# Kernel optimization log

Measured on AMD Instinct MI355X. Metric: run time of the kernel, lower is better.

The kernel has to match this reference:

```python
import jax, jax.numpy as jnp
import numpy as np

EMBED, HEADS, LEVELS, POINTS = 256, 8, 3, 4
HD = EMBED // HEADS
SHAPES = [(200, 200), (100, 100), (50, 50)]


def layer_norm(x, g, b, eps=1e-5):
    m = x.mean(-1, keepdims=True)
    v = ((x - m) ** 2).mean(-1, keepdims=True)
    return (x - m) * jax.lax.rsqrt(v + eps) * g + b


def bilinear_sample(v, loc, H, W):
    """v: (bs, H*W, heads, hd); loc: (bs, nq, heads, P, 2) normalized to [0,1].
    Matches F.grid_sample(bilinear, align_corners=False, padding_mode='zeros')
    applied to grid = 2*loc - 1. Returns (bs, nq, heads, P, hd)."""
    bs, nq, heads, P, _ = loc.shape
    hd = v.shape[-1]
    x = loc[..., 0] * W - 0.5
    y = loc[..., 1] * H - 0.5
    x0 = jnp.floor(x); y0 = jnp.floor(y)
    tx = x - x0; ty = y - y0
    x0i = x0.astype(jnp.int32); y0i = y0.astype(jnp.int32)
    vT = v.transpose(0, 2, 1, 3)  # (bs, heads, HW, hd)
    out = jnp.zeros((bs, heads, nq * P, hd), v.dtype)
    for dy, wy in ((0, 1.0 - ty), (1, ty)):
        for dx, wx in ((0, 1.0 - tx), (1, tx)):
            xi = x0i + dx; yi = y0i + dy
            valid = (xi >= 0) & (xi < W) & (yi >= 0) & (yi < H)
            idx = jnp.clip(yi, 0, H - 1) * W + jnp.clip(xi, 0, W - 1)
            w = (wx * wy * valid).transpose(0, 2, 1, 3).reshape(bs, heads, nq * P)
            idxT = idx.transpose(0, 2, 1, 3).reshape(bs, heads, nq * P)
            g = jnp.take_along_axis(vT, idxT[..., None], axis=2)  # (bs,heads,nqP,hd)
            out = out + w[..., None] * g
    return out.reshape(bs, heads, nq, P, hd).transpose(0, 2, 1, 3, 4)


def reference(query, value, query_pos, ref_pts, spatial_shapes, level_start_index,
              norm1_g, norm1_b, W_off, b_off, W_attn, b_attn, W_val, b_val,
              W_out, b_out, norm2_g, norm2_b, W1, b1, W2, b2):
    shapes = np.asarray(spatial_shapes)
    bs, nq, _ = query.shape
    # --- MultiScaleDeformableAttention on norm1(query) ---
    q = layer_norm(query, norm1_g, norm1_b)
    identity = q
    qp = q + query_pos
    offsets = (qp @ W_off + b_off).reshape(bs, nq, HEADS, LEVELS, POINTS, 2)
    aw = (qp @ W_attn + b_attn).reshape(bs, nq, HEADS, LEVELS * POINTS)
    aw = jax.nn.softmax(aw, axis=-1).reshape(bs, nq, HEADS, LEVELS, POINTS)
    v = (value @ W_val + b_val).reshape(bs, -1, HEADS, HD)
    # offset normalizer is (W, H) per level
    normalizer = jnp.stack([spatial_shapes[:, 1], spatial_shapes[:, 0]], -1).astype(query.dtype)
    loc = ref_pts[:, :, None, :, None, :] + offsets / normalizer[None, None, None, :, None, :]
    out = jnp.zeros((bs, nq, HEADS, HD), query.dtype)
    start = 0
    for l in range(LEVELS):
        H, W = int(shapes[l, 0]), int(shapes[l, 1])
        vl = v[:, start:start + H * W]
        s = bilinear_sample(vl, loc[:, :, :, l], H, W)  # (bs,nq,heads,P,hd)
        out = out + jnp.einsum('bqhpd,bqhp->bqhd', s, aw[:, :, :, l])
        start += H * W
    attn_out = out.reshape(bs, nq, EMBED) @ W_out + b_out + identity
    x = query + attn_out
    # --- FFN ---
    h = layer_norm(x, norm2_g, norm2_b)
    ffn = jax.nn.gelu(h @ W1 + b1, approximate=False) @ W2 + b2
    return x + ffn


def setup_inputs() -> dict:
    key = jax.random.key(0)
    ks = jax.random.split(key, 16)
    bs, nq = 1, 40000
    nv = sum(h * w for h, w in SHAPES)
    d = EMBED
    inp = {
        'query': jax.random.normal(ks[0], (bs, nq, d), jnp.float32),
        'value': jax.random.normal(ks[1], (bs, nv, d), jnp.float32),
        'query_pos': jax.random.normal(ks[2], (bs, nq, d), jnp.float32),
        'ref_pts': jax.random.uniform(ks[3], (bs, nq, LEVELS, 2), jnp.float32),
        'spatial_shapes': jnp.array(SHAPES, dtype=jnp.int32),
        'level_start_index': jnp.array(np.cumsum([0] + [h * w for h, w in SHAPES[:-1]]), dtype=jnp.int32),
    }
    s = 1.0 / np.sqrt(d)
    inp.update({
        'norm1_g': jnp.ones((d,), jnp.float32), 'norm1_b': jnp.zeros((d,), jnp.float32),
        'W_off': jax.random.normal(ks[4], (d, HEADS * LEVELS * POINTS * 2), jnp.float32) * 0.01,
        'b_off': jax.random.normal(ks[5], (HEADS * LEVELS * POINTS * 2,), jnp.float32) * 0.5,
        'W_attn': jax.random.normal(ks[6], (d, HEADS * LEVELS * POINTS), jnp.float32) * s,
        'b_attn': jnp.zeros((HEADS * LEVELS * POINTS,), jnp.float32),
        'W_val': jax.random.normal(ks[7], (d, d), jnp.float32) * s,
        'b_val': jnp.zeros((d,), jnp.float32),
        'W_out': jax.random.normal(ks[8], (d, d), jnp.float32) * s,
        'b_out': jnp.zeros((d,), jnp.float32),
        'norm2_g': jnp.ones((d,), jnp.float32), 'norm2_b': jnp.zeros((d,), jnp.float32),
        'W1': jax.random.normal(ks[9], (d, 4 * d), jnp.float32) * s,
        'b1': jnp.zeros((4 * d,), jnp.float32),
        'W2': jax.random.normal(ks[10], (4 * d, d), jnp.float32) / np.sqrt(4 * d),
        'b2': jnp.zeros((d,), jnp.float32),
    })
    return inp
```

## Files before the change

kernel.cpp:

```cpp
#include <hip/hip_runtime.h>
#include <hip/hip_bf16.h>
#include <math.h>

#define NQ 40000
#define NV 52500
#define D 256
#define NHEAD 8
#define HD 32
#define GUARD 256

using bf16x8 = __attribute__((ext_vector_type(8))) short;
using f32x4  = __attribute__((ext_vector_type(4))) float;
typedef int v2i32 __attribute__((ext_vector_type(2)));

__device__ __forceinline__ short f2bf(float f) {
  union { __hip_bfloat16 h; short s; } u;
  u.h = __float2bfloat16(f);
  return u.s;
}
__device__ __forceinline__ float bf2f(unsigned short s) {
  return __uint_as_float((unsigned)s << 16);
}
__device__ __forceinline__ unsigned pack2(float lo, float hi) {
  return (unsigned)(unsigned short)f2bf(lo) |
         ((unsigned)(unsigned short)f2bf(hi) << 16);
}
__device__ __forceinline__ void gload16(const void* g, void* l) {
  __builtin_amdgcn_global_load_lds(
      (const __attribute__((address_space(1))) unsigned int*)g,
      (__attribute__((address_space(3))) unsigned int*)l, 16, 0, 0);
}

template<int IMM>
__device__ __forceinline__ float swz_add(float x) {
  return x + __int_as_float(__builtin_amdgcn_ds_swizzle(__float_as_int(x), IMM));
}
__device__ __forceinline__ float xor16_add(float x) {
#if __has_builtin(__builtin_amdgcn_permlane16_swap)
  v2i32 r = __builtin_amdgcn_permlane16_swap(__float_as_int(x), __float_as_int(x), false, false);
  return __int_as_float(r[0]) + __int_as_float(r[1]);
#else
  return x + __shfl_xor(x, 16);
#endif
}
__device__ __forceinline__ float xor32_add(float x) {
#if __has_builtin(__builtin_amdgcn_permlane32_swap)
  v2i32 r = __builtin_amdgcn_permlane32_swap(__float_as_int(x), __float_as_int(x), false, false);
  return __int_as_float(r[0]) + __int_as_float(r[1]);
#else
  return x + __shfl_xor(x, 32);
#endif
}

__global__ __launch_bounds__(256) void k_wt(const float* __restrict__ Wm,
                                            short* __restrict__ WT, int K, int N) {
  int idx = blockIdx.x * 256 + threadIdx.x;
  if (idx >= N * K) return;
  int n = idx / K, k = idx - n * K;
  WT[idx] = f2bf(Wm[(size_t)k * N + n]);
}

__global__ void k_catbias(const float* __restrict__ a, const float* __restrict__ b,
                          float* __restrict__ o) {
  int i = threadIdx.x;
  if (i < 192) o[i] = a[i];
  else if (i < 288) o[i] = b[i - 192];
}

__global__ __launch_bounds__(256) void k_ln1(const float* __restrict__ qin,
                                             const float* __restrict__ qpos,
                                             const float* __restrict__ g,
                                             const float* __restrict__ b,
                                             float* __restrict__ id_out,
                                             short* __restrict__ qp_out) {
  int wave = threadIdx.x >> 6;
  int lane = threadIdx.x & 63;
  int row  = blockIdx.x * 4 + wave;
  float4 x = ((const float4*)(qin + (size_t)row * D))[lane];
  float s  = x.x + x.y + x.z + x.w;
  float ss = x.x*x.x + x.y*x.y + x.z*x.z + x.w*x.w;
  for (int o = 32; o > 0; o >>= 1) { s += __shfl_down(s, o); ss += __shfl_down(ss, o); }
  s  = __shfl(s, 0);
  ss = __shfl(ss, 0);
  float m   = s * (1.0f / 256.0f);
  float var = ss * (1.0f / 256.0f) - m * m;
  float rs  = rsqrtf(var + 1e-5f);
  float4 gg = ((const float4*)g)[lane];
  float4 bb = ((const float4*)b)[lane];
  float4 qn;
  qn.x = (x.x - m) * rs * gg.x + bb.x;
  qn.y = (x.y - m) * rs * gg.y + bb.y;
  qn.z = (x.z - m) * rs * gg.z + bb.z;
  qn.w = (x.w - m) * rs * gg.w + bb.w;
  ((float4*)(id_out + (size_t)row * D))[lane] = qn;
  float4 p = ((const float4*)(qpos + (size_t)row * D))[lane];
  short4 o;
  o.x = f2bf(qn.x + p.x); o.y = f2bf(qn.y + p.y);
  o.z = f2bf(qn.z + p.z); o.w = f2bf(qn.w + p.w);
  ((short4*)(qp_out + (size_t)row * D))[lane] = o;
}

__global__ __launch_bounds__(256) void k_ln2(const float* __restrict__ xin,
                                             const float* __restrict__ g,
                                             const float* __restrict__ b,
                                             short* __restrict__ h_out) {
  int wave = threadIdx.x >> 6;
  int lane = threadIdx.x & 63;
  int row  = blockIdx.x * 4 + wave;
  float4 x = ((const float4*)(xin + (size_t)row * D))[lane];
  float s  = x.x + x.y + x.z + x.w;
  float ss = x.x*x.x + x.y*x.y + x.z*x.z + x.w*x.w;
  for (int o = 32; o > 0; o >>= 1) { s += __shfl_down(s, o); ss += __shfl_down(ss, o); }
  s  = __shfl(s, 0);
  ss = __shfl(ss, 0);
  float m   = s * (1.0f / 256.0f);
  float var = ss * (1.0f / 256.0f) - m * m;
  float rs  = rsqrtf(var + 1e-5f);
  float4 gg = ((const float4*)g)[lane];
  float4 bb = ((const float4*)b)[lane];
  short4 o;
  o.x = f2bf((x.x - m) * rs * gg.x + bb.x);
  o.y = f2bf((x.y - m) * rs * gg.y + bb.y);
  o.z = f2bf((x.z - m) * rs * gg.z + bb.z);
  o.w = f2bf((x.w - m) * rs * gg.w + bb.w);
  ((short4*)(h_out + (size_t)row * D))[lane] = o;
}

template<int EPI, int CVTA, int K>
__global__ __launch_bounds__(256) void k_gemm(const void* __restrict__ Ain,
                                              const short* __restrict__ WT,
                                              const float* __restrict__ bias,
                                              float* __restrict__ Cf,
                                              short* __restrict__ Cb,
                                              const float* __restrict__ R1,
                                              const float* __restrict__ R2,
                                              int M, int N) {
  constexpr int NT = K / 32;
  __shared__ short Al[3][4096];
  __shared__ short Bl[3][4096];
  const int tid = threadIdx.x;

  const int nbx = gridDim.x;
  const int nwg = nbx * gridDim.y;
  int flat = blockIdx.y * nbx + blockIdx.x;
  {
    int xcd = flat & 7, pos = flat >> 3;
    int qq = nwg >> 3, rr = nwg & 7;
    flat = (xcd < rr ? xcd * (qq + 1) : rr * (qq + 1) + (xcd - rr) * qq) + pos;
  }
  const int n0 = (flat % nbx) * 128, m0 = (flat / nbx) * 128;

  const int w = tid >> 6, l = tid & 63;
  const int wm = (w >> 1) * 64, wn = (w & 1) * 64;
  const int lr = l & 15;

  const int c0s = w * 2, c1s = c0s + 1;
  const int sr = l >> 2;
  const int sg = (((l & 3) ^ ((l >> 3) & 3)) << 3);
  const int ar0 = min(m0 + c0s * 16 + sr, M - 1);
  const int ar1 = min(m0 + c1s * 16 + sr, M - 1);
  const int br0 = min(n0 + c0s * 16 + sr, N - 1);
  const int br1 = min(n0 + c1s * 16 + sr, N - 1);
  const short* bP0 = WT + (size_t)br0 * K + sg;
  const short* bP1 = WT + (size_t)br1 * K + sg;
  const short* aP0 = (const short*)Ain + (size_t)ar0 * K + sg;
  const short* aP1 = (const short*)Ain + (size_t)ar1 * K + sg;
  const float* aF0 = (const float*)Ain + (size_t)ar0 * K + sg;
  const float* aF1 = (const float*)Ain + (size_t)ar1 * K + sg;
  short* wD0 = &Al[0][(c0s * 16 + sr) * 32 + ((l & 3) << 3)];
  short* wD1 = &Al[0][(c1s * 16 + sr) * 32 + ((l & 3) << 3)];

  const int fsw = (((l >> 4) ^ ((l >> 1) & 3)) << 3);
  const int aRd = (wm + lr) * 32 + fsw;
  const int bRd = (wn + lr) * 32 + fsw;

  f32x4 acc[4][4];
#pragma unroll
  for (int i = 0; i < 4; ++i)
#pragma unroll
    for (int j = 0; j < 4; ++j) acc[i][j] = (f32x4){0, 0, 0, 0};

  if (CVTA) {
    {
      float4 f00 = *(const float4*)(aF0);
      float4 f01 = *(const float4*)(aF0 + 4);
      float4 f10 = *(const float4*)(aF1);
      float4 f11 = *(const float4*)(aF1 + 4);
      int4 p0, p1;
      p0.x = pack2(f00.x, f00.y); p0.y = pack2(f00.z, f00.w);
      p0.z = pack2(f01.x, f01.y); p0.w = pack2(f01.z, f01.w);
      p1.x = pack2(f10.x, f10.y); p1.y = pack2(f10.z, f10.w);
      p1.z = pack2(f11.x, f11.y); p1.w = pack2(f11.z, f11.w);
      *(int4*)wD0 = p0;
      *(int4*)wD1 = p1;
      gload16(bP0, &Bl[0][c0s * 512]);
      gload16(bP1, &Bl[0][c1s * 512]);
      __syncthreads();
    }
#pragma unroll 2
    for (int t = 0; t < NT - 1; ++t) {
      const int buf = t & 1, nbuf = buf ^ 1;
      const int kn = (t + 1) * 32;
      float4 f00 = *(const float4*)(aF0 + kn);
      float4 f01 = *(const float4*)(aF0 + kn + 4);
      float4 f10 = *(const float4*)(aF1 + kn);
      float4 f11 = *(const float4*)(aF1 + kn + 4);
      gload16(bP0 + kn, &Bl[nbuf][c0s * 512]);
      gload16(bP1 + kn, &Bl[nbuf][c1s * 512]);

      bf16x8 af[4], bfr[4];
#pragma unroll
      for (int i = 0; i < 4; ++i) {
        af[i]  = *(const bf16x8*)&Al[buf][aRd + i * 512];
        bfr[i] = *(const bf16x8*)&Bl[buf][bRd + i * 512];
      }
#pragma unroll
      for (int i = 0; i < 4; ++i)
#pragma unroll
        for (int j = 0; j < 4; ++j)
          acc[i][j] = __builtin_amdgcn_mfma_f32_16x16x32_bf16(af[i], bfr[j], acc[i][j], 0, 0, 0);

      int4 p0, p1;
      p0.x = pack2(f00.x, f00.y); p0.y = pack2(f00.z, f00.w);
      p0.z = pack2(f01.x, f01.y); p0.w = pack2(f01.z, f01.w);
      p1.x = pack2(f10.x, f10.y); p1.y = pack2(f10.z, f10.w);
      p1.z = pack2(f11.x, f11.y); p1.w = pack2(f11.z, f11.w);
      *(int4*)(wD0 + nbuf * 4096) = p0;
      *(int4*)(wD1 + nbuf * 4096) = p1;
      __syncthreads();
    }
    {
      const int buf = (NT - 1) & 1;
      bf16x8 af[4], bfr[4];
#pragma unroll
      for (int i = 0; i < 4; ++i) {
        af[i]  = *(const bf16x8*)&Al[buf][aRd + i * 512];
        bfr[i] = *(const bf16x8*)&Bl[buf][bRd + i * 512];
      }
#pragma unroll
      for (int i = 0; i < 4; ++i)
#pragma unroll
        for (int j = 0; j < 4; ++j)
          acc[i][j] = __builtin_amdgcn_mfma_f32_16x16x32_bf16(af[i], bfr[j], acc[i][j], 0, 0, 0);
    }
  } else {
    gload16(aP0, &Al[0][c0s * 512]);
    gload16(aP1, &Al[0][c1s * 512]);
    gload16(bP0, &Bl[0][c0s * 512]);
    gload16(bP1, &Bl[0][c1s * 512]);
    if (NT > 1) {
      gload16(aP0 + 32, &Al[1][c0s * 512]);
      gload16(aP1 + 32, &Al[1][c1s * 512]);
      gload16(bP0 + 32, &Bl[1][c0s * 512]);
      gload16(bP1 + 32, &Bl[1][c1s * 512]);
    }
#pragma unroll
    for (int t = 0; t < NT; ++t) {
      const int buf = t % 3;
      if (t + 1 < NT) asm volatile("s_waitcnt vmcnt(4)" ::: "memory");
      else            asm volatile("s_waitcnt vmcnt(0)" ::: "memory");
      __builtin_amdgcn_s_barrier();
      __builtin_amdgcn_sched_barrier(0);
      if (t + 2 < NT) {
        const int kn = (t + 2) * 32, nb = (t + 2) % 3;
        gload16(aP0 + kn, &Al[nb][c0s * 512]);
        gload16(aP1 + kn, &Al[nb][c1s * 512]);
        gload16(bP0 + kn, &Bl[nb][c0s * 512]);
        gload16(bP1 + kn, &Bl[nb][c1s * 512]);
      }
      bf16x8 af[4], bfr[4];
#pragma unroll
      for (int i = 0; i < 4; ++i) {
        af[i]  = *(const bf16x8*)&Al[buf][aRd + i * 512];
        bfr[i] = *(const bf16x8*)&Bl[buf][bRd + i * 512];
      }
#pragma unroll
      for (int i = 0; i < 4; ++i)
#pragma unroll
        for (int j = 0; j < 4; ++j)
          acc[i][j] = __builtin_amdgcn_mfma_f32_16x16x32_bf16(af[i], bfr[j], acc[i][j], 0, 0, 0);
    }
  }

  __syncthreads();
  float* scratch = (float*)&Al[0][0];
  const int wrow = (w >> 1) * 16;
  const int rl2 = tid >> 3;
  const int cc0 = (tid & 7) * 16;
  const bool colok = (n0 + cc0) < N;
  float bsv[16];
#pragma unroll
  for (int c = 0; c < 4; ++c) {
    float4 bv = {0, 0, 0, 0};
    if (colok) bv = *(const float4*)&bias[n0 + cc0 + c * 4];
    bsv[c*4+0] = bv.x; bsv[c*4+1] = bv.y; bsv[c*4+2] = bv.z; bsv[c*4+3] = bv.w;
  }
#pragma unroll
  for (int i = 0; i < 4; ++i) {
#pragma unroll
    for (int j = 0; j < 4; ++j) {
      const int col = wn + j * 16 + (l & 15);
      const int rbase = wrow + ((l >> 4) << 2);
#pragma unroll
      for (int r = 0; r < 4; ++r)
        scratch[(rbase + r) * 140 + col] = acc[i][j][r];
    }
    __syncthreads();
    const int grow = m0 + 16 * i + (rl2 < 16 ? rl2 : 48 + rl2);
    if (colok && grow < M) {
      const size_t base = (size_t)grow * N + n0 + cc0;
      float v16[16];
#pragma unroll
      for (int c = 0; c < 4; ++c) {
        float4 vv = *(const float4*)&scratch[rl2 * 140 + cc0 + c * 4];
        v16[c*4+0] = vv.x + bsv[c*4+0];
        v16[c*4+1] = vv.y + bsv[c*4+1];
        v16[c*4+2] = vv.z + bsv[c*4+2];
        v16[c*4+3] = vv.w + bsv[c*4+3];
      }
      if (EPI == 0) {
#pragma unroll
        for (int c = 0; c < 4; ++c)
          *(float4*)&Cf[base + c * 4] =
              (float4){v16[c*4], v16[c*4+1], v16[c*4+2], v16[c*4+3]};
      } else if (EPI == 1) {
        uint4 o0, o1;
        unsigned pk[8];
#pragma unroll
        for (int c = 0; c < 8; ++c) {
          float a0 = v16[2*c], a1 = v16[2*c+1];
          float u0 = a0 * (2.3021178f + 0.1029445f * a0 * a0);
          float u1 = a1 * (2.3021178f + 0.1029445f * a1 * a1);
          float g0 = a0 - a0 / (1.0f + exp2f(u0));
          float g1 = a1 - a1 / (1.0f + exp2f(u1));
          pk[c] = pack2(g0, g1);
        }
        o0 = (uint4){pk[0], pk[1], pk[2], pk[3]};
        o1 = (uint4){pk[4], pk[5], pk[6], pk[7]};
        *(uint4*)&Cb[base] = o0;
        *(uint4*)&Cb[base + 8] = o1;
      } else if (EPI == 2) {
#pragma unroll
        for (int c = 0; c < 4; ++c) {
          float4 r1 = *(const float4*)&R1[base + c * 4];
          float4 r2 = *(const float4*)&R2[base + c * 4];
          *(float4*)&Cf[base + c * 4] =
              (float4){v16[c*4] + r1.x + r2.x, v16[c*4+1] + r1.y + r2.y,
                       v16[c*4+2] + r1.z + r2.z, v16[c*4+3] + r1.w + r2.w};
        }
      } else if (EPI == 3) {
#pragma unroll
        for (int c = 0; c < 4; ++c) {
          float4 cur = *(const float4*)&Cf[base + c * 4];
          *(float4*)&Cf[base + c * 4] =
              (float4){cur.x + v16[c*4], cur.y + v16[c*4+1],
                       cur.z + v16[c*4+2], cur.w + v16[c*4+3]};
        }
      } else {
        uint4 o0 = (uint4){pack2(v16[0], v16[1]), pack2(v16[2], v16[3]),
                           pack2(v16[4], v16[5]), pack2(v16[6], v16[7])};
        uint4 o1 = (uint4){pack2(v16[8], v16[9]), pack2(v16[10], v16[11]),
                           pack2(v16[12], v16[13]), pack2(v16[14], v16[15])};
        *(uint4*)&Cb[base] = o0;
        *(uint4*)&Cb[base + 8] = o1;
      }
    }
    __syncthreads();
  }
}

__global__ __launch_bounds__(256) void k_post(const unsigned short* __restrict__ res,
                                              const float* __restrict__ refp,
                                              int* __restrict__ idxA,
                                              unsigned short* __restrict__ wA) {
  int t = blockIdx.x * 256 + threadIdx.x;
  if (t >= NQ * 8) return;
  int q = t >> 3, h = t & 7;
  const unsigned short* rr = res + (size_t)q * 288;
  const unsigned short* lg = rr + 192 + h * 12;
  float lf[12];
#pragma unroll
  for (int i = 0; i < 12; ++i) lf[i] = bf2f(lg[i]);
  float mx = lf[0];
#pragma unroll
  for (int i = 1; i < 12; ++i) mx = fmaxf(mx, lf[i]);
  float e[12]; float sum = 0.0f;
#pragma unroll
  for (int i = 0; i < 12; ++i) { e[i] = expf(lf[i] - mx); sum += e[i]; }
  float inv = 1.0f / sum;

  const float dims[3] = {200.0f, 100.0f, 50.0f};
  const int   sts[3]  = {0, 40000, 50000};
#pragma unroll
  for (int l = 0; l < 3; ++l) {
    const int W = (int)dims[l];
    const float fW = dims[l];
    float rx = refp[((size_t)q * 3 + l) * 2 + 0];
    float ry = refp[((size_t)q * 3 + l) * 2 + 1];
    float invd = 1.0f / fW;
#pragma unroll
    for (int p = 0; p < 4; ++p) {
      int j = ((h * 3 + l) * 4 + p) * 2;
      float lx = rx + bf2f(rr[j + 0]) * invd;
      float ly = ry + bf2f(rr[j + 1]) * invd;
      float fx = lx * fW - 0.5f;
      float fy = ly * fW - 0.5f;
      float x0f = floorf(fx), y0f = floorf(fy);
      float tx = fx - x0f, ty = fy - y0f;
      int x0 = (int)x0f, y0 = (int)y0f;
      bool vx0 = (unsigned)x0       < (unsigned)W;
      bool vx1 = (unsigned)(x0 + 1) < (unsigned)W;
      bool vy0 = (unsigned)y0       < (unsigned)W;
      bool vy1 = (unsigned)(y0 + 1) < (unsigned)W;
      float a = e[l * 4 + p] * inv;
      float w00 = (vx0 && vy0) ? a * (1.0f - tx) * (1.0f - ty) : 0.0f;
      float w01 = (vx1 && vy0) ? a * tx * (1.0f - ty) : 0.0f;
      float w10 = (vx0 && vy1) ? a * (1.0f - tx) * ty : 0.0f;
      float w11 = (vx1 && vy1) ? a * tx * ty : 0.0f;
      int pidx = t * 12 + l * 4 + p;
      idxA[pidx] = sts[l] + y0 * W + x0;
      short4 wpk;
      wpk.x = f2bf(w00); wpk.y = f2bf(w01);
      wpk.z = f2bf(w10); wpk.w = f2bf(w11);
      *(short4*)(wA + (size_t)pidx * 4) = wpk;
    }
  }
}

__global__ __launch_bounds__(256) void k_sample(const short* __restrict__ vprojG,
                                                const int* __restrict__ idxA,
                                                const unsigned short* __restrict__ wA,
                                                short* __restrict__ smp) {
  const int lane = threadIdx.x & 63;
  const int qh   = blockIdx.x * 4 + (threadIdx.x >> 6);
  const int h = qh & 7;
  const int pg  = lane >> 4;
  const int tap = (lane >> 2) & 3;
  const int cq  = lane & 3;
  const int dy = tap >> 1, dx = tap & 1;
  const short* vb = vprojG + (size_t)GUARD * D + h * HD + cq * 8;

  float acc[8];
#pragma unroll
  for (int j = 0; j < 8; ++j) acc[j] = 0.0f;

  const int Dim[3] = {200, 100, 50};
#pragma unroll
  for (int l = 0; l < 3; ++l) {
    const int W = Dim[l];
    const int tapoff = dy * W + dx;
    int pidx = qh * 12 + l * 4 + pg;
    int idx = idxA[pidx] + tapoff;
    float wgt = __uint_as_float((unsigned)wA[(size_t)pidx * 4 + tap] << 16);
    uint4 v = *(const uint4*)(vb + (ptrdiff_t)idx * D);
    acc[0] = fmaf(wgt, __uint_as_float(v.x << 16),        acc[0]);
    acc[1] = fmaf(wgt, __uint_as_float(v.x & 0xffff0000u), acc[1]);
    acc[2] = fmaf(wgt, __uint_as_float(v.y << 16),        acc[2]);
    acc[3] = fmaf(wgt, __uint_as_float(v.y & 0xffff0000u), acc[3]);
    acc[4] = fmaf(wgt, __uint_as_float(v.z << 16),        acc[4]);
    acc[5] = fmaf(wgt, __uint_as_float(v.z & 0xffff0000u), acc[5]);
    acc[6] = fmaf(wgt, __uint_as_float(v.w << 16),        acc[6]);
    acc[7] = fmaf(wgt, __uint_as_float(v.w & 0xffff0000u), acc[7]);
  }

#pragma unroll
  for (int j = 0; j < 8; ++j) {
    float a = swz_add<0x101F>(acc[j]);
    a = swz_add<0x201F>(a);
    a = xor16_add(a);
    acc[j] = xor32_add(a);
  }

  if (lane < 4) {
    uint4 o;
    o.x = pack2(acc[0], acc[1]);
    o.y = pack2(acc[2], acc[3]);
    o.z = pack2(acc[4], acc[5]);
    o.w = pack2(acc[6], acc[7]);
    *(uint4*)(smp + (size_t)qh * HD + cq * 8) = o;
  }
}

extern "C" void kernel_launch(void* const* d_in, const int* in_sizes, int n_in,
                              void* d_out, int out_size, void* d_ws, size_t ws_size,
                              hipStream_t stream) {
  const float* query  = (const float*)d_in[0];
  const float* value  = (const float*)d_in[1];
  const float* qpos   = (const float*)d_in[2];
  const float* refp   = (const float*)d_in[3];
  const float* n1g = (const float*)d_in[6];
  const float* n1b = (const float*)d_in[7];
  const float* Woff = (const float*)d_in[8];
  const float* boff = (const float*)d_in[9];
  const float* Wattn = (const float*)d_in[10];
  const float* battn = (const float*)d_in[11];
  const float* Wval = (const float*)d_in[12];
  const float* bval = (const float*)d_in[13];
  const float* Wout = (const float*)d_in[14];
  const float* bout = (const float*)d_in[15];
  const float* n2g = (const float*)d_in[16];
  const float* n2b = (const float*)d_in[17];
  const float* W1 = (const float*)d_in[18];
  const float* b1 = (const float*)d_in[19];
  const float* W2 = (const float*)d_in[20];
  const float* b2 = (const float*)d_in[21];

  float* out = (float*)d_out;
  char* Wb = (char*)d_ws;

  short* qp_bf   = (short*)Wb;
  float* iden    = (float*)(Wb + 20480000);
  int*   idxA    = (int*)(Wb + 61440000);
  unsigned short* wA = (unsigned short*)(Wb + 76800000);
  short* res_bf  = (short*)(Wb + 107520000);
  short* vprjG   = (short*)(Wb + 107520000);
  short* vprj_bf = (short*)(Wb + 107520000 + GUARD * D * 2);
  short* h_bf    = (short*)(Wb + 107520000);
  short* smp_bf  = (short*)(Wb + 134662144);
  short* mid_bf  = (short*)Wb;
  char*  Wbase   = Wb + 155142144;
  short* WT288   = (short*)(Wbase);
  short* WTval   = (short*)(Wbase + 147456);
  short* WTout   = (short*)(Wbase + 278528);
  short* WT1     = (short*)(Wbase + 409600);
  short* WT2     = (short*)(Wbase + 933888);
  float* bias288 = (float*)(Wbase + 1458176);

  k_wt<<<(192 * 256 + 255) / 256, 256, 0, stream>>>(Woff, WT288, 256, 192);
  k_wt<<<(96 * 256 + 255) / 256, 256, 0, stream>>>(Wattn, WT288 + 192 * 256, 256, 96);
  k_wt<<<(256 * 256 + 255) / 256, 256, 0, stream>>>(Wval, WTval, 256, 256);
  k_wt<<<(256 * 256 + 255) / 256, 256, 0, stream>>>(Wout, WTout, 256, 256);
  k_wt<<<(1024 * 256 + 255) / 256, 256, 0, stream>>>(W1, WT1, 256, 1024);
  k_wt<<<(256 * 1024 + 255) / 256, 256, 0, stream>>>(W2, WT2, 1024, 256);
  k_catbias<<<1, 320, 0, stream>>>(boff, battn, bias288);

  k_ln1<<<NQ / 4, 256, 0, stream>>>(query, qpos, n1g, n1b, iden, qp_bf);

  k_gemm<4,0,256><<<dim3(3, (NQ + 127) / 128), 256, 0, stream>>>(
      qp_bf, WT288, bias288, nullptr, res_bf, nullptr, nullptr, NQ, 288);
  k_post<<<(NQ * 8 + 255) / 256, 256, 0, stream>>>(
      (const unsigned short*)res_bf, refp, idxA, wA);

  k_gemm<4,1,256><<<dim3(2, (NV + 127) / 128), 256, 0, stream>>>(
      value, WTval, bval, nullptr, vprj_bf, nullptr, nullptr, NV, 256);

  k_sample<<<NQ * NHEAD / 4, 256, 0, stream>>>(vprjG, idxA, wA, smp_bf);

  k_gemm<2,0,256><<<dim3(2, (NQ + 127) / 128), 256, 0, stream>>>(
      smp_bf, WTout, bout, out, nullptr, query, iden, NQ, 256);

  k_ln2<<<NQ / 4, 256, 0, stream>>>(out, n2g, n2b, h_bf);

  k_gemm<1,0,256><<<dim3(8, (NQ + 127) / 128), 256, 0, stream>>>(
      h_bf, WT1, b1, nullptr, mid_bf, nullptr, nullptr, NQ, 1024);

  k_gemm<3,0,1024><<<dim3(2, (NQ + 127) / 128), 256, 0, stream>>>(
      mid_bf, WT2, b2, out, nullptr, nullptr, nullptr, NQ, 256);
}
```

Measured before the change: 379.3 us.

## Merge weight prep kernels, store identity as bf16, and restructure sampling lanes

The six weight-transpose launches and the bias-concat launch become one k_prep launch, which cuts launch overhead. The LayerNorm identity is now stored as bf16 instead of fp32, and a new GEMM epilogue (EPI 5) reads it back as bf16. This halves that residual's write and read traffic but adds rounding error to the residual path. The sampling kernel now gives each 16-lane group one query-head that loops over all 12 points, instead of spreading points across lane groups, so it needs only the two swizzle reductions and no permlane reductions.

```diff
diff --git a/kernel.cpp b/kernel.cpp
--- a/kernel.cpp
+++ b/kernel.cpp
@@ -35,43 +35,51 @@
 __device__ __forceinline__ float swz_add(float x) {
   return x + __int_as_float(__builtin_amdgcn_ds_swizzle(__float_as_int(x), IMM));
 }
-__device__ __forceinline__ float xor16_add(float x) {
-#if __has_builtin(__builtin_amdgcn_permlane16_swap)
-  v2i32 r = __builtin_amdgcn_permlane16_swap(__float_as_int(x), __float_as_int(x), false, false);
-  return __int_as_float(r[0]) + __int_as_float(r[1]);
-#else
-  return x + __shfl_xor(x, 16);
-#endif
-}
-__device__ __forceinline__ float xor32_add(float x) {
-#if __has_builtin(__builtin_amdgcn_permlane32_swap)
-  v2i32 r = __builtin_amdgcn_permlane32_swap(__float_as_int(x), __float_as_int(x), false, false);
-  return __int_as_float(r[0]) + __int_as_float(r[1]);
-#else
-  return x + __shfl_xor(x, 32);
-#endif
-}
-
-__global__ __launch_bounds__(256) void k_wt(const float* __restrict__ Wm,
-                                            short* __restrict__ WT, int K, int N) {
+
+__global__ __launch_bounds__(256) void k_prep(const float* __restrict__ Woff,
+                                              const float* __restrict__ Wattn,
+                                              const float* __restrict__ Wval,
+                                              const float* __restrict__ Wout,
+                                              const float* __restrict__ W1,
+                                              const float* __restrict__ W2,
+                                              const float* __restrict__ boff,
+                                              const float* __restrict__ battn,
+                                              short* __restrict__ WT288,
+                                              short* __restrict__ WTval,
+                                              short* __restrict__ WTout,
+                                              short* __restrict__ WT1,
+                                              short* __restrict__ WT2,
+                                              float* __restrict__ bias288) {
   int idx = blockIdx.x * 256 + threadIdx.x;
-  if (idx >= N * K) return;
-  int n = idx / K, k = idx - n * K;
-  WT[idx] = f2bf(Wm[(size_t)k * N + n]);
-}
-
-__global__ void k_catbias(const float* __restrict__ a, const float* __restrict__ b,
-                          float* __restrict__ o) {
-  int i = threadIdx.x;
-  if (i < 192) o[i] = a[i];
-  else if (i < 288) o[i] = b[i - 192];
+  if (idx < 49152) {
+    int n = idx >> 8, k = idx & 255;
+    WT288[idx] = f2bf(Woff[k * 192 + n]);
+  } else if (idx < 73728) {
+    int li = idx - 49152; int n = li >> 8, k = li & 255;
+    WT288[49152 + li] = f2bf(Wattn[k * 96 + n]);
+  } else if (idx < 139264) {
+    int li = idx - 73728; int n = li >> 8, k = li & 255;
+    WTval[li] = f2bf(Wval[k * 256 + n]);
+  } else if (idx < 204800) {
+    int li = idx - 139264; int n = li >> 8, k = li & 255;
+    WTout[li] = f2bf(Wout[k * 256 + n]);
+  } else if (idx < 466944) {
+    int li = idx - 204800; int n = li >> 8, k = li & 255;
+    WT1[li] = f2bf(W1[k * 1024 + n]);
+  } else if (idx < 729088) {
+    int li = idx - 466944; int n = li >> 10, k = li & 1023;
+    WT2[li] = f2bf(W2[k * 256 + n]);
+  } else if (idx < 729376) {
+    int i = idx - 729088;
+    bias288[i] = (i < 192) ? boff[i] : battn[i - 192];
+  }
 }
 
 __global__ __launch_bounds__(256) void k_ln1(const float* __restrict__ qin,
                                              const float* __restrict__ qpos,
                                              const float* __restrict__ g,
                                              const float* __restrict__ b,
-                                             float* __restrict__ id_out,
+                                             short* __restrict__ id_out,
                                              short* __restrict__ qp_out) {
   int wave = threadIdx.x >> 6;
   int lane = threadIdx.x & 63;
@@ -92,7 +100,9 @@
   qn.y = (x.y - m) * rs * gg.y + bb.y;
   qn.z = (x.z - m) * rs * gg.z + bb.z;
   qn.w = (x.w - m) * rs * gg.w + bb.w;
-  ((float4*)(id_out + (size_t)row * D))[lane] = qn;
+  short4 io;
+  io.x = f2bf(qn.x); io.y = f2bf(qn.y); io.z = f2bf(qn.z); io.w = f2bf(qn.w);
+  ((short4*)(id_out + (size_t)row * D))[lane] = io;
   float4 p = ((const float4*)(qpos + (size_t)row * D))[lane];
   short4 o;
   o.x = f2bf(qn.x + p.x); o.y = f2bf(qn.y + p.y);
@@ -284,6 +294,7 @@
 
   __syncthreads();
   float* scratch = (float*)&Al[0][0];
+  const unsigned short* R2b = (const unsigned short*)R2;
   const int wrow = (w >> 1) * 16;
   const int rl2 = tid >> 3;
   const int cc0 = (tid & 7) * 16;
@@ -324,7 +335,6 @@
           *(float4*)&Cf[base + c * 4] =
               (float4){v16[c*4], v16[c*4+1], v16[c*4+2], v16[c*4+3]};
       } else if (EPI == 1) {
-        uint4 o0, o1;
         unsigned pk[8];
 #pragma unroll
         for (int c = 0; c < 8; ++c) {
@@ -335,18 +345,24 @@
           float g1 = a1 - a1 / (1.0f + exp2f(u1));
           pk[c] = pack2(g0, g1);
         }
-        o0 = (uint4){pk[0], pk[1], pk[2], pk[3]};
-        o1 = (uint4){pk[4], pk[5], pk[6], pk[7]};
-        *(uint4*)&Cb[base] = o0;
-        *(uint4*)&Cb[base + 8] = o1;
-      } else if (EPI == 2) {
+        *(uint4*)&Cb[base] = (uint4){pk[0], pk[1], pk[2], pk[3]};
+        *(uint4*)&Cb[base + 8] = (uint4){pk[4], pk[5], pk[6], pk[7]};
+      } else if (EPI == 5) {
+        uint4 rb0 = *(const uint4*)&R2b[base];
+        uint4 rb1 = *(const uint4*)&R2b[base + 8];
+        unsigned rw[8] = {rb0.x, rb0.y, rb0.z, rb0.w, rb1.x, rb1.y, rb1.z, rb1.w};
+        float r2v[16];
+#pragma unroll
+        for (int c = 0; c < 8; ++c) {
+          r2v[2*c]   = __uint_as_float(rw[c] << 16);
+          r2v[2*c+1] = __uint_as_float(rw[c] & 0xffff0000u);
+        }
 #pragma unroll
         for (int c = 0; c < 4; ++c) {
           float4 r1 = *(const float4*)&R1[base + c * 4];
-          float4 r2 = *(const float4*)&R2[base + c * 4];
           *(float4*)&Cf[base + c * 4] =
-              (float4){v16[c*4] + r1.x + r2.x, v16[c*4+1] + r1.y + r2.y,
-                       v16[c*4+2] + r1.z + r2.z, v16[c*4+3] + r1.w + r2.w};
+              (float4){v16[c*4] + r1.x + r2v[c*4], v16[c*4+1] + r1.y + r2v[c*4+1],
+                       v16[c*4+2] + r1.z + r2v[c*4+2], v16[c*4+3] + r1.w + r2v[c*4+3]};
         }
       } else if (EPI == 3) {
 #pragma unroll
@@ -432,13 +448,13 @@
                                                 const unsigned short* __restrict__ wA,
                                                 short* __restrict__ smp) {
   const int lane = threadIdx.x & 63;
-  const int qh   = blockIdx.x * 4 + (threadIdx.x >> 6);
+  const int qh   = blockIdx.x * 16 + (threadIdx.x >> 6) * 4 + (lane >> 4);
+  const int tap  = (lane >> 2) & 3;
+  const int cq   = lane & 3;
   const int h = qh & 7;
-  const int pg  = lane >> 4;
-  const int tap = (lane >> 2) & 3;
-  const int cq  = lane & 3;
   const int dy = tap >> 1, dx = tap & 1;
   const short* vb = vprojG + (size_t)GUARD * D + h * HD + cq * 8;
+  const int pbase = qh * 12;
 
   float acc[8];
 #pragma unroll
@@ -446,12 +462,12 @@
 
   const int Dim[3] = {200, 100, 50};
 #pragma unroll
-  for (int l = 0; l < 3; ++l) {
-    const int W = Dim[l];
+  for (int it = 0; it < 12; ++it) {
+    const int W = Dim[it >> 2];
     const int tapoff = dy * W + dx;
-    int pidx = qh * 12 + l * 4 + pg;
+    int pidx = pbase + it;
     int idx = idxA[pidx] + tapoff;
-    float wgt = __uint_as_float((unsigned)wA[(size_t)pidx * 4 + tap] << 16);
+    float wgt = bf2f(wA[(size_t)pidx * 4 + tap]);
     uint4 v = *(const uint4*)(vb + (ptrdiff_t)idx * D);
     acc[0] = fmaf(wgt, __uint_as_float(v.x << 16),        acc[0]);
     acc[1] = fmaf(wgt, __uint_as_float(v.x & 0xffff0000u), acc[1]);
@@ -466,12 +482,10 @@
 #pragma unroll
   for (int j = 0; j < 8; ++j) {
     float a = swz_add<0x101F>(acc[j]);
-    a = swz_add<0x201F>(a);
-    a = xor16_add(a);
-    acc[j] = xor32_add(a);
-  }
-
-  if (lane < 4) {
+    acc[j] = swz_add<0x201F>(a);
+  }
+
+  if (tap == 0) {
     uint4 o;
     o.x = pack2(acc[0], acc[1]);
     o.y = pack2(acc[2], acc[3]);
@@ -509,7 +523,7 @@
   char* Wb = (char*)d_ws;
 
   short* qp_bf   = (short*)Wb;
-  float* iden    = (float*)(Wb + 20480000);
+  short* iden_bf = (short*)(Wb + 20480000);
   int*   idxA    = (int*)(Wb + 61440000);
   unsigned short* wA = (unsigned short*)(Wb + 76800000);
   short* res_bf  = (short*)(Wb + 107520000);
@@ -526,15 +540,11 @@
   short* WT2     = (short*)(Wbase + 933888);
   float* bias288 = (float*)(Wbase + 1458176);
 
-  k_wt<<<(192 * 256 + 255) / 256, 256, 0, stream>>>(Woff, WT288, 256, 192);
-  k_wt<<<(96 * 256 + 255) / 256, 256, 0, stream>>>(Wattn, WT288 + 192 * 256, 256, 96);
-  k_wt<<<(256 * 256 + 255) / 256, 256, 0, stream>>>(Wval, WTval, 256, 256);
-  k_wt<<<(256 * 256 + 255) / 256, 256, 0, stream>>>(Wout, WTout, 256, 256);
-  k_wt<<<(1024 * 256 + 255) / 256, 256, 0, stream>>>(W1, WT1, 256, 1024);
-  k_wt<<<(256 * 1024 + 255) / 256, 256, 0, stream>>>(W2, WT2, 1024, 256);
-  k_catbias<<<1, 320, 0, stream>>>(boff, battn, bias288);
-
-  k_ln1<<<NQ / 4, 256, 0, stream>>>(query, qpos, n1g, n1b, iden, qp_bf);
+  k_prep<<<(729376 + 255) / 256, 256, 0, stream>>>(
+      Woff, Wattn, Wval, Wout, W1, W2, boff, battn,
+      WT288, WTval, WTout, WT1, WT2, bias288);
+
+  k_ln1<<<NQ / 4, 256, 0, stream>>>(query, qpos, n1g, n1b, iden_bf, qp_bf);
 
   k_gemm<4,0,256><<<dim3(3, (NQ + 127) / 128), 256, 0, stream>>>(
       qp_bf, WT288, bias288, nullptr, res_bf, nullptr, nullptr, NQ, 288);
@@ -544,10 +554,10 @@
   k_gemm<4,1,256><<<dim3(2, (NV + 127) / 128), 256, 0, stream>>>(
       value, WTval, bval, nullptr, vprj_bf, nullptr, nullptr, NV, 256);
 
-  k_sample<<<NQ * NHEAD / 4, 256, 0, stream>>>(vprjG, idxA, wA, smp_bf);
-
-  k_gemm<2,0,256><<<dim3(2, (NQ + 127) / 128), 256, 0, stream>>>(
-      smp_bf, WTout, bout, out, nullptr, query, iden, NQ, 256);
+  k_sample<<<NQ * NHEAD / 16, 256, 0, stream>>>(vprjG, idxA, wA, smp_bf);
+
+  k_gemm<5,0,256><<<dim3(2, (NQ + 127) / 128), 256, 0, stream>>>(
+      smp_bf, WTout, bout, out, nullptr, query, (const float*)iden_bf, NQ, 256);
 
   k_ln2<<<NQ / 4, 256, 0, stream>>>(out, n2g, n2b, h_bf);
 
```

Measured after the change: 362.3 us. 4.5% less time.
